# Performance work log

Measured on AMD Instinct MI355X. Metric: run time of the kernel, lower is better.

## Reference

```python
import jax, jax.numpy as jnp
import numpy as np

B, N, C = 4, 4096, 512
K = 683  # ceil(N / ratio=6.0)
TAU = 1.0
W_OCC, W_REP, W_ENT = 1.0, 0.1, 0.01
REP_TOPK, REP_MARGIN = 4, -1.0
NEG = -1e9


def setup_inputs() -> dict:
    key = jax.random.key(0)
    ks = jax.random.split(key, 5)
    s = jax.random.normal(ks[0], (B, N, C), jnp.float32)
    mu = jax.random.normal(ks[1], (B, N, 3), jnp.float32)
    # SPD covariance per residue: L L^T + 0.1 I
    L = jax.random.normal(ks[2], (B, N, 3, 3), jnp.float32) * 0.3
    Sigma = jnp.einsum('bnij,bnkj->bnik', L, L) + 0.1 * jnp.eye(3, dtype=jnp.float32)
    mask = jnp.ones((B, N), jnp.float32)
    W = jax.random.normal(ks[3], (C, C), jnp.float32) / np.sqrt(C).astype(np.float32)
    b = jnp.zeros((C,), jnp.float32)
    slots = jax.random.normal(ks[4], (K, C), jnp.float32) * 0.02
    return {"s": s, "mu": mu, "Sigma": Sigma, "mask": mask, "W": W, "b": b, "slots": slots}


def reference(s, mu, Sigma, mask, W, b, slots):
    Kk = slots.shape[0]
    # A = softmax((Linear(s)) . slots / tau), masked
    s_proj = jnp.einsum('bnc,dc->bnd', s, W) + b            # nn.Linear: x @ W^T + b
    logits = jnp.einsum('bnc,kc->bnk', s_proj, slots) / TAU
    logits = jnp.where((mask < 0.5)[..., None], NEG, logits)
    A = jax.nn.softmax(logits, axis=-1) * mask[..., None]   # [B,N,K]

    denom = jnp.maximum(A.sum(axis=1), 1e-8)                # [B,K]
    s_c = jnp.einsum('bnk,bnc->bkc', A, s) / denom[..., None]

    # moment-matching merge
    w = A / (A.sum(axis=1, keepdims=True) + 1e-8)           # [B,N,K]
    mu_c = jnp.einsum('bnk,bnd->bkd', w, mu)                # [B,K,3]
    intra = jnp.einsum('bnk,bnij->bkij', w, Sigma)          # [B,K,3,3]
    diff = mu[:, :, None, :] - mu_c[:, None, :, :]          # [B,N,K,3]
    inter = jnp.einsum('bnk,bnki,bnkj->bkij', w, diff, diff)
    Sigma_c = intra + inter                                 # [B,K,3,3]

    # occupancy balance loss
    occ = A.sum(axis=1)
    occ = occ / jnp.maximum(occ.sum(axis=-1, keepdims=True), 1e-8)
    loss_occ = jnp.mean((occ - 1.0 / Kk) ** 2)

    # repulsion loss (pairwise Gaussian overlap)
    delta = mu_c[:, :, None, :] - mu_c[:, None, :, :]       # [B,K,K,3]
    sig_sum = Sigma_c[:, :, None] + Sigma_c[:, None, :]     # [B,K,K,3,3]
    inv = jnp.linalg.inv(sig_sum + 1e-6 * jnp.eye(3, dtype=s.dtype))
    dist2 = jnp.einsum('bpqi,bpqij,bpqj->bpq', delta, inv, delta)
    score = -0.5 * dist2
    eye = jnp.eye(Kk, dtype=bool)[None]
    score = jnp.where(eye, NEG, score)
    top = jax.lax.top_k(score, min(REP_TOPK, Kk - 1))[0]
    loss_rep = jnp.mean(jax.nn.relu(top - REP_MARGIN))

    # entropy loss
    Ac = jnp.maximum(A, 1e-8)
    ent = -(Ac * jnp.log(Ac)).sum(axis=-1)                  # [B,N]
    loss_ent = (ent * mask).sum() / jnp.maximum(mask.sum(), 1.0)

    total = W_OCC * loss_occ + W_REP * loss_rep + W_ENT * loss_ent
    return (A, s_c, mu_c, Sigma_c, loss_occ, loss_rep, loss_ent, total)
```

## Files before the change

kernel.cpp:

```cpp
#include <hip/hip_runtime.h>
#include <math.h>

#define B_    4
#define N_    4096
#define C_    512
#define KSLOT 683

using bf16x8 = __attribute__((ext_vector_type(8))) short;
using f32x4  = __attribute__((ext_vector_type(4))) float;

#define OFF_A    0
#define OFF_SC   (B_*N_*KSLOT)
#define OFF_MU   (OFF_SC + B_*KSLOT*C_)
#define OFF_SIG  (OFF_MU + B_*KSLOT*3)
#define OFF_LOSS (OFF_SIG + B_*KSLOT*9)

#define WS_MOM    0
#define WS_INVMAX (WS_MOM + B_*KSLOT*16)
#define WS_OCCTB  (WS_INVMAX + B_*KSLOT)
#define WS_OCCT   (WS_OCCTB + 256)
#define WS_ENTB   (WS_OCCT + 4)
#define WS_MSB    (WS_ENTB + 256)
#define WS_OCCLB  (WS_MSB + 256)
#define WS_REPB   (WS_OCCLB + 256)
#define WS_BS     (WS_REPB + 256)
#define WS_FEND   (WS_BS + 704)

#define US_BASE  (WS_FEND*2)
#define US_SBF   US_BASE
#define US_STF   (US_SBF + B_*N_*C_)
#define US_WSL   (US_STF + B_*C_*N_)
#define US_FT    (US_WSL + 704*C_)
#define US_ATB   (US_FT + B_*16*N_)
#define US_END   (US_ATB + (size_t)B_*768*N_)


__device__ __forceinline__ ushort f2bf(float x) {
  union { float f; unsigned u; } v; v.f = x;
  unsigned r = v.u + 0x7fffu + ((v.u >> 16) & 1u);
  return (ushort)(r >> 16);
}

__device__ __forceinline__ float blockSum256(float v, float* red) {
#pragma unroll
  for (int off = 32; off; off >>= 1) v += __shfl_xor(v, off);
  __syncthreads();
  if ((threadIdx.x & 63) == 0) red[threadIdx.x >> 6] = v;
  __syncthreads();
  return red[0] + red[1] + red[2] + red[3];
}

__device__ __forceinline__ void top4_insert(float v, float& t0, float& t1, float& t2, float& t3) {
  if (v > t3) {
    if (v > t2) {
      t3 = t2;
      if (v > t1) {
        t2 = t1;
        if (v > t0) { t1 = t0; t0 = v; } else t1 = v;
      } else t2 = v;
    } else t3 = v;
  }
}

__global__ __launch_bounds__(256) void convert_s_kernel(const float* __restrict__ s,
                                                        ushort* __restrict__ sbf,
                                                        ushort* __restrict__ stf) {
  __shared__ float T[32][33];
  const int b = blockIdx.z;
  const int n0 = blockIdx.x * 32, c0 = blockIdx.y * 32;
  const int t = threadIdx.x;
  const int r = t >> 3, q4 = (t & 7) * 4;
  float4 v = *(const float4*)(s + ((size_t)(b * N_ + n0 + r)) * C_ + c0 + q4);
  ushort4 u;
  u.x = f2bf(v.x); u.y = f2bf(v.y); u.z = f2bf(v.z); u.w = f2bf(v.w);
  *(ushort4*)(sbf + ((size_t)(b * N_ + n0 + r)) * C_ + c0 + q4) = u;
  T[q4 + 0][r] = v.x; T[q4 + 1][r] = v.y; T[q4 + 2][r] = v.z; T[q4 + 3][r] = v.w;
  __syncthreads();
  ushort4 o;
  o.x = f2bf(T[r][q4 + 0]); o.y = f2bf(T[r][q4 + 1]);
  o.z = f2bf(T[r][q4 + 2]); o.w = f2bf(T[r][q4 + 3]);
  *(ushort4*)(stf + ((size_t)(b * C_ + c0 + r)) * N_ + n0 + q4) = o;
}

__global__ __launch_bounds__(256) void build_features_t(const float* __restrict__ mu,
                                                        const float* __restrict__ Sig,
                                                        ushort* __restrict__ ftg) {
  __shared__ ushort FT[16][272];
  const int t = threadIdx.x;
  const size_t ng = (size_t)blockIdx.x * 256 + t;
  const float* mp = mu + ng * 3;
  const float* sp = Sig + ng * 9;
  float m0 = mp[0], m1 = mp[1], m2 = mp[2];
  FT[0][t] = 0x3F80;
  FT[1][t] = f2bf(m0); FT[2][t] = f2bf(m1); FT[3][t] = f2bf(m2);
  FT[4][t] = f2bf(m0 * m0); FT[5][t] = f2bf(m0 * m1); FT[6][t] = f2bf(m0 * m2);
  FT[7][t] = f2bf(m1 * m1); FT[8][t] = f2bf(m1 * m2); FT[9][t] = f2bf(m2 * m2);
  FT[10][t] = f2bf(sp[0]); FT[11][t] = f2bf(sp[1]); FT[12][t] = f2bf(sp[2]);
  FT[13][t] = f2bf(sp[4]); FT[14][t] = f2bf(sp[5]); FT[15][t] = f2bf(sp[8]);
  __syncthreads();
  const int b = (int)((blockIdx.x * 256) >> 12);
  const int n0b = (blockIdx.x * 256) & (N_ - 1);
  for (int u = t; u < 512; u += 256) {
    int f = u >> 5, off = (u & 31) * 8;
    *(uint4*)(ftg + ((size_t)b * 16 + f) * N_ + n0b + off) = *(uint4*)(&FT[f][off]);
  }
}

__global__ __launch_bounds__(256) void wslots_bf16_kernel(const float* __restrict__ slots,
                                                          const float* __restrict__ W,
                                                          ushort* __restrict__ wsl) {
  __shared__ float SL[8][512];
  const int k0 = blockIdx.x * 8;
  const int c = blockIdx.y * 256 + threadIdx.x;
  for (int idx = threadIdx.x; idx < 8 * 512; idx += 256) {
    int kk = idx >> 9, d = idx & 511;
    SL[kk][d] = (k0 + kk < KSLOT) ? slots[(size_t)(k0 + kk) * C_ + d] : 0.f;
  }
  __syncthreads();
  float acc[8];
#pragma unroll
  for (int i = 0; i < 8; ++i) acc[i] = 0.f;
  for (int d = 0; d < C_; ++d) {
    float w = W[(size_t)d * C_ + c];
#pragma unroll
    for (int i = 0; i < 8; ++i) acc[i] += SL[i][d] * w;
  }
#pragma unroll
  for (int i = 0; i < 8; ++i)
    if (k0 + i < KSLOT) wsl[(size_t)(k0 + i) * C_ + c] = f2bf(acc[i]);
}

__global__ __launch_bounds__(256) void bs_kernel(const float* __restrict__ slots,
                                                 const float* __restrict__ bvec,
                                                 float* __restrict__ bs) {
  int k = blockIdx.x * 256 + threadIdx.x;
  if (k >= KSLOT) return;
  const float* srow = slots + (size_t)k * C_;
  float acc = 0.f;
  for (int d = 0; d < C_; ++d) acc += srow[d] * bvec[d];
  bs[k] = acc;
}

__device__ __forceinline__ void g1_epilogue(
    f32x4 (&acc)[11], const int rowbase, const int t, const int lane,
    const int rowg, const int colw,
    const float* __restrict__ bs, const float* __restrict__ mask,
    float* __restrict__ Aout, ushort* __restrict__ atb,
    float* __restrict__ entb, float* __restrict__ msb,
    float* Af, float (&red4)[32][4], const int binid) {
  __syncthreads();
  int cols[11]; bool valid[11];
#pragma unroll
  for (int cf = 0; cf < 11; ++cf) {
    cols[cf] = colw * 176 + cf * 16 + (lane & 15);
    valid[cf] = (cols[cf] < KSLOT);
    float bv = valid[cf] ? bs[cols[cf]] : 0.f;
#pragma unroll
    for (int r = 0; r < 4; ++r) acc[cf][r] += bv;
  }
  float m4[4];
#pragma unroll
  for (int r = 0; r < 4; ++r) m4[r] = -3.0e38f;
#pragma unroll
  for (int cf = 0; cf < 11; ++cf)
    if (valid[cf]) {
#pragma unroll
      for (int r = 0; r < 4; ++r) m4[r] = fmaxf(m4[r], acc[cf][r]);
    }
#pragma unroll
  for (int off = 1; off < 16; off <<= 1) {
#pragma unroll
    for (int r = 0; r < 4; ++r) m4[r] = fmaxf(m4[r], __shfl_xor(m4[r], off));
  }
  if ((lane & 15) == 0) {
#pragma unroll
    for (int r = 0; r < 4; ++r) red4[rowg * 16 + (lane >> 4) * 4 + r][colw] = m4[r];
  }
  __syncthreads();
#pragma unroll
  for (int r = 0; r < 4; ++r) {
    int rl = rowg * 16 + (lane >> 4) * 4 + r;
    m4[r] = fmaxf(fmaxf(red4[rl][0], red4[rl][1]), fmaxf(red4[rl][2], red4[rl][3]));
  }
  __syncthreads();
  float s4[4] = {0.f, 0.f, 0.f, 0.f};
#pragma unroll
  for (int cf = 0; cf < 11; ++cf)
    if (valid[cf]) {
#pragma unroll
      for (int r = 0; r < 4; ++r) {
        float e = __expf(acc[cf][r] - m4[r]);
        acc[cf][r] = e;
        s4[r] += e;
      }
    }
#pragma unroll
  for (int off = 1; off < 16; off <<= 1) {
#pragma unroll
    for (int r = 0; r < 4; ++r) s4[r] += __shfl_xor(s4[r], off);
  }
  if ((lane & 15) == 0) {
#pragma unroll
    for (int r = 0; r < 4; ++r) red4[rowg * 16 + (lane >> 4) * 4 + r][colw] = s4[r];
  }
  __syncthreads();
  float inv4[4], mr4[4];
#pragma unroll
  for (int r = 0; r < 4; ++r) {
    int rl = rowg * 16 + (lane >> 4) * 4 + r;
    float S = red4[rl][0] + red4[rl][1] + red4[rl][2] + red4[rl][3];
    inv4[r] = 1.f / S;
    mr4[r] = mask[rowbase + rl];
  }
  __syncthreads();
  float ent4[4] = {0.f, 0.f, 0.f, 0.f};
#pragma unroll
  for (int cf = 0; cf < 11; ++cf)
    if (valid[cf]) {
#pragma unroll
      for (int r = 0; r < 4; ++r) {
        int rl = rowg * 16 + (lane >> 4) * 4 + r;
        float a = acc[cf][r] * inv4[r] * mr4[r];
        Af[rl * KSLOT + cols[cf]] = a;
        float ac = fmaxf(a, 1e-8f);
        ent4[r] -= ac * __logf(ac);
      }
    }
#pragma unroll
  for (int off = 1; off < 16; off <<= 1) {
#pragma unroll
    for (int r = 0; r < 4; ++r) ent4[r] += __shfl_xor(ent4[r], off);
  }
  if ((lane & 15) == 0) {
#pragma unroll
    for (int r = 0; r < 4; ++r) red4[rowg * 16 + (lane >> 4) * 4 + r][colw] = ent4[r];
  }
  __syncthreads();
  if (t < 64) {
    float er = 0.f, ms = 0.f;
    if (t < 32) {
      float e = red4[t][0] + red4[t][1] + red4[t][2] + red4[t][3];
      float m = mask[rowbase + t];
      er = e * m; ms = m;
    }
#pragma unroll
    for (int off = 32; off; off >>= 1) { er += __shfl_xor(er, off); ms += __shfl_xor(ms, off); }
    if (t == 0) {
      atomicAdd(&entb[binid], er);
      atomicAdd(&msb[binid], ms);
    }
  }
  const float4* Af4 = (const float4*)Af;
  float4* Ag4 = (float4*)(Aout + (size_t)rowbase * KSLOT);
  for (int i = t; i < (32 * KSLOT) / 4; i += 512) Ag4[i] = Af4[i];
  {
    const int bb = rowbase >> 12;
    const int n0b = rowbase & (N_ - 1);
    ushort* Atb = atb + ((size_t)bb * 768) * N_ + n0b;
    for (int u = t; u < KSLOT * 4; u += 512) {
      int k = u >> 2, q = u & 3;
      ushort tmp[8];
#pragma unroll
      for (int j = 0; j < 8; ++j) tmp[j] = f2bf(Af[(q * 8 + j) * KSLOT + k]);
      *(uint4*)(Atb + (size_t)k * N_ + q * 8) = *(uint4*)tmp;
    }
  }
}

__global__ __launch_bounds__(512)
__attribute__((amdgpu_waves_per_eu(2, 2)))
void gemm1sm(const ushort* __restrict__ sbf,
             const ushort* __restrict__ wsl,
             const float* __restrict__ bs,
             const float* __restrict__ mask,
             float* __restrict__ Aout,
             ushort* __restrict__ atb,
             float* __restrict__ entb,
             float* __restrict__ msb) {
  __shared__ __align__(16) char SMEM[90112];
  float* Af = (float*)SMEM;
  __shared__ float red4[32][4];
  const int t = threadIdx.x;
  const int lane = t & 63;
  const int w = t >> 6;
  const int rowg = w >> 2;
  const int colw = w & 3;
  const int row0 = blockIdx.x * 64;
  const int r16 = rowg * 16 + (lane & 15);

  const ushort* arow0 = sbf + (size_t)(row0 + r16) * C_ + (lane >> 4) * 8;
  const ushort* arow1 = arow0 + (size_t)32 * C_;
  bf16x8 g0a = *(const bf16x8*)(arow0);
  bf16x8 g0b = *(const bf16x8*)(arow0 + 32);
  bf16x8 g1a = *(const bf16x8*)(arow1);
  bf16x8 g1b = *(const bf16x8*)(arow1 + 32);
  bf16x8 p0a, p0b, p1a, p1b;

  f32x4 acc0[11], acc1[11];
  f32x4 zero = {0.f, 0.f, 0.f, 0.f};
#pragma unroll
  for (int cf = 0; cf < 11; ++cf) { acc0[cf] = zero; acc1[cf] = zero; }

#pragma unroll
  for (int slab = 0; slab < 8; ++slab) {
    if (slab) __syncthreads();
#pragma unroll
    for (int i = 0; i < 11; ++i) {
      int idx = t + i * 512;
      int r = idx >> 3;
      int chs = (idx & 7) ^ (r & 7);
      const ushort* g = wsl + (size_t)r * C_ + slab * 64 + chs * 8;
      char* l = (char*)SMEM + i * 8192 + (t & 448) * 16;
      __builtin_amdgcn_global_load_lds(
          (const __attribute__((address_space(1))) void*)g,
          (__attribute__((address_space(3))) void*)l, 16, 0, 0);
    }
    __syncthreads();
    if (slab < 7) {
      p0a = *(const bf16x8*)(arow0 + (slab + 1) * 64);
      p0b = *(const bf16x8*)(arow0 + (slab + 1) * 64 + 32);
      p1a = *(const bf16x8*)(arow1 + (slab + 1) * 64);
      p1b = *(const bf16x8*)(arow1 + (slab + 1) * 64 + 32);
    }
    {
      const int ach0 = (lane >> 4);
#pragma unroll
      for (int cf = 0; cf < 11; ++cf) {
        int br = colw * 176 + cf * 16 + (lane & 15);
        bf16x8 bf = *(const bf16x8*)(SMEM + br * 128 + ((ach0 * 16) ^ ((br & 7) << 4)));
        acc0[cf] = __builtin_amdgcn_mfma_f32_16x16x32_bf16(g0a, bf, acc0[cf], 0, 0, 0);
        acc1[cf] = __builtin_amdgcn_mfma_f32_16x16x32_bf16(g1a, bf, acc1[cf], 0, 0, 0);
      }
      const int ach1 = 4 + (lane >> 4);
#pragma unroll
      for (int cf = 0; cf < 11; ++cf) {
        int br = colw * 176 + cf * 16 + (lane & 15);
        bf16x8 bf = *(const bf16x8*)(SMEM + br * 128 + ((ach1 * 16) ^ ((br & 7) << 4)));
        acc0[cf] = __builtin_amdgcn_mfma_f32_16x16x32_bf16(g0b, bf, acc0[cf], 0, 0, 0);
        acc1[cf] = __builtin_amdgcn_mfma_f32_16x16x32_bf16(g1b, bf, acc1[cf], 0, 0, 0);
      }
    }
    g0a = p0a; g0b = p0b; g1a = p1a; g1b = p1b;
  }

  g1_epilogue(acc0, row0, t, lane, rowg, colw, bs, mask, Aout, atb, entb, msb,
              Af, red4, (blockIdx.x * 2) & 255);
  g1_epilogue(acc1, row0 + 32, t, lane, rowg, colw, bs, mask, Aout, atb, entb, msb,
              Af, red4, (blockIdx.x * 2 + 1) & 255);
}

#define G2BUFB 18432
__global__ __launch_bounds__(256) void gemm2t(const ushort* __restrict__ atb,
                                              const ushort* __restrict__ stf,
                                              const ushort* __restrict__ ftg,
                                              float* __restrict__ sc,
                                              float* __restrict__ MOM) {
  __shared__ __align__(16) char LB[2 * G2BUFB];
  const int t = threadIdx.x;
  const int lane = t & 63;
  const int w = t >> 6;
  const int wm = w >> 1;
  const int wn = w & 1;
  const int fhw = blockIdx.x;
  const int logical = (fhw & 7) * 44 + (fhw >> 3);
  const int kt = logical % 11;
  const int ct = (logical / 11) & 7;
  const int b  = logical / 88;
  const bool do_mom = (ct == 0);
  const ushort* Ab = atb + ((size_t)b * 768 + kt * 64) * N_;
  const ushort* Sb = stf + ((size_t)b * C_ + ct * 64) * N_;
  const ushort* Fb = ftg + ((size_t)b * 16) * N_;

  f32x4 zero = {0.f, 0.f, 0.f, 0.f};
  f32x4 acc[2][2];
#pragma unroll
  for (int i = 0; i < 2; ++i)
#pragma unroll
    for (int j = 0; j < 2; ++j) acc[i][j] = zero;
  f32x4 accf[2];
#pragma unroll
  for (int i = 0; i < 2; ++i) accf[i] = zero;

#define G2_STAGE(BUFI, NB)                                                   \
  {                                                                          \
    char* AtL = LB + (BUFI) * G2BUFB;                                        \
    char* SsL = AtL + 8192;                                                  \
    char* FtL = AtL + 16384;                                                 \
    _Pragma("unroll")                                                        \
    for (int i = 0; i < 2; ++i) {                                            \
      int idx = t + i * 256;                                                 \
      int r = idx >> 3;                                                      \
      int chs = (idx & 7) ^ (r & 7);                                         \
      const ushort* g = Ab + (size_t)r * N_ + (NB) + chs * 8;                \
      char* l = AtL + i * 4096 + (t & 192) * 16;                             \
      __builtin_amdgcn_global_load_lds(                                      \
          (const __attribute__((address_space(1))) void*)g,                  \
          (__attribute__((address_space(3))) void*)l, 16, 0, 0);             \
    }                                                                        \
    _Pragma("unroll")                                                        \
    for (int i = 0; i < 2; ++i) {                                            \
      int idx = t + i * 256;                                                 \
      int r = idx >> 3;                                                      \
      int chs = (idx & 7) ^ (r & 7);                                         \
      const ushort* g = Sb + (size_t)r * N_ + (NB) + chs * 8;                \
      char* l = SsL + i * 4096 + (t & 192) * 16;                             \
      __builtin_amdgcn_global_load_lds(                                      \
          (const __attribute__((address_space(1))) void*)g,                  \
          (__attribute__((address_space(3))) void*)l, 16, 0, 0);             \
    }                                                                        \
    if (do_mom && t < 128) {                                                 \
      int idx = t;                                                           \
      int r = idx >> 3;                                                      \
      int chs = (idx & 7) ^ (r & 7);                                         \
      const ushort* g = Fb + (size_t)r * N_ + (NB) + chs * 8;                \
      char* l = FtL + (t & 192) * 16;                                        \
      __builtin_amdgcn_global_load_lds(                                      \
          (const __attribute__((address_space(1))) void*)g,                  \
          (__attribute__((address_space(3))) void*)l, 16, 0, 0);             \
    }                                                                        \
  }

  G2_STAGE(0, 0)
  for (int st = 0; st < 64; ++st) {
    const int cur = st & 1;
    __syncthreads();
    if (st < 63) G2_STAGE(cur ^ 1, (st + 1) * 64)
    char* AtL = LB + cur * G2BUFB;
    char* SsL = AtL + 8192;
    char* FtL = AtL + 16384;
#pragma unroll
    for (int ks2 = 0; ks2 < 2; ++ks2) {
      const int ach = ks2 * 4 + (lane >> 4);
      bf16x8 afr[2], bfr[2];
#pragma unroll
      for (int kf = 0; kf < 2; ++kf) {
        int ar = wm * 32 + kf * 16 + (lane & 15);
        afr[kf] = *(const bf16x8*)(AtL + ar * 128 + ((ach * 16) ^ ((ar & 7) << 4)));
      }
#pragma unroll
      for (int cg = 0; cg < 2; ++cg) {
        int br = wn * 32 + cg * 16 + (lane & 15);
        bfr[cg] = *(const bf16x8*)(SsL + br * 128 + ((ach * 16) ^ ((br & 7) << 4)));
      }
#pragma unroll
      for (int kf = 0; kf < 2; ++kf)
#pragma unroll
        for (int cg = 0; cg < 2; ++cg)
          acc[kf][cg] = __builtin_amdgcn_mfma_f32_16x16x32_bf16(afr[kf], bfr[cg], acc[kf][cg], 0, 0, 0);
      if (do_mom && wn == 0) {
        int fr = lane & 15;
        bf16x8 ffr = *(const bf16x8*)(FtL + fr * 128 + ((ach * 16) ^ ((fr & 7) << 4)));
#pragma unroll
        for (int kf = 0; kf < 2; ++kf)
          accf[kf] = __builtin_amdgcn_mfma_f32_16x16x32_bf16(afr[kf], ffr, accf[kf], 0, 0, 0);
      }
    }
  }
#undef G2_STAGE

#pragma unroll
  for (int kf = 0; kf < 2; ++kf) {
#pragma unroll
    for (int r = 0; r < 4; ++r) {
      int k = kt * 64 + wm * 32 + kf * 16 + (lane >> 4) * 4 + r;
      if (k >= KSLOT) continue;
      float* dst = sc + ((size_t)(b * KSLOT + k)) * C_ + ct * 64 + wn * 32;
#pragma unroll
      for (int cg = 0; cg < 2; ++cg)
        dst[cg * 16 + (lane & 15)] = acc[kf][cg][r];
    }
  }
  if (do_mom && wn == 0) {
#pragma unroll
    for (int kf = 0; kf < 2; ++kf) {
#pragma unroll
      for (int r = 0; r < 4; ++r) {
        int k = kt * 64 + wm * 32 + kf * 16 + (lane >> 4) * 4 + r;
        if (k >= KSLOT) continue;
        MOM[((size_t)b * KSLOT + k) * 16 + (lane & 15)] = accf[kf][r];
      }
    }
  }
}

__global__ __launch_bounds__(128) void scale_sc(float* __restrict__ sc,
                                                const float* __restrict__ invmax) {
  const int bk = blockIdx.x;
  const float sv = invmax[bk];
  float4* p = (float4*)(sc + (size_t)bk * C_);
  int t = threadIdx.x;
  float4 v = p[t];
  v.x *= sv; v.y *= sv; v.z *= sv; v.w *= sv;
  p[t] = v;
}

__global__ __launch_bounds__(256) void moments_kernel(const float* __restrict__ Amat,
                                                      const float* __restrict__ mu,
                                                      const float* __restrict__ Sig,
                                                      float* __restrict__ MOM) {
  __shared__ float red[64][17];
  const int b = blockIdx.z;
  const int kx = threadIdx.x & 63;
  const int k = blockIdx.x * 64 + kx;
  const int ng = threadIdx.x >> 6;
  const int n0 = blockIdx.y * 128;
  const bool valid = (k < KSLOT);

  float acc[16];
#pragma unroll
  for (int i = 0; i < 16; ++i) acc[i] = 0.f;

  const float* Abase = Amat + (size_t)b * N_ * KSLOT + k;
  const float* mubase = mu + ((size_t)b * N_) * 3;
  const float* sgbase = Sig + ((size_t)b * N_) * 9;

  for (int j = 0; j < 32; ++j) {
    const int n = n0 + ng + j * 4;
    float a = valid ? Abase[(size_t)n * KSLOT] : 0.f;
    const float* mp = mubase + (size_t)n * 3;
    const float* sp = sgbase + (size_t)n * 9;
    float m0 = mp[0], m1 = mp[1], m2 = mp[2];
    acc[0] += a;
    acc[1] += a * m0; acc[2] += a * m1; acc[3] += a * m2;
    acc[4] += a * m0 * m0; acc[5] += a * m0 * m1; acc[6] += a * m0 * m2;
    acc[7] += a * m1 * m1; acc[8] += a * m1 * m2; acc[9] += a * m2 * m2;
    acc[10] += a * sp[0]; acc[11] += a * sp[1]; acc[12] += a * sp[2];
    acc[13] += a * sp[4]; acc[14] += a * sp[5]; acc[15] += a * sp[8];
  }

  if (ng == 0) {
#pragma unroll
    for (int i = 0; i < 16; ++i) red[kx][i] = acc[i];
  }
  __syncthreads();
  if (ng == 1) {
#pragma unroll
    for (int i = 0; i < 16; ++i) red[kx][i] += acc[i];
  }
  __syncthreads();
  if (ng == 2) {
#pragma unroll
    for (int i = 0; i < 16; ++i) red[kx][i] += acc[i];
  }
  __syncthreads();
  if (ng == 3) {
#pragma unroll
    for (int i = 0; i < 16; ++i) red[kx][i] += acc[i];
  }
  __syncthreads();
  if (ng == 0 && valid) {
    float* dst = MOM + ((size_t)b * KSLOT + k) * 16;
#pragma unroll
    for (int i = 0; i < 16; ++i) atomicAdd(&dst[i], red[kx][i]);
  }
}

__global__ __launch_bounds__(256) void finalize_bk(const float* __restrict__ MOM,
                                                   float* __restrict__ muc,
                                                   float* __restrict__ sigc,
                                                   float* __restrict__ invmax,
                                                   float* __restrict__ occtb) {
  int bk = blockIdx.x * 256 + threadIdx.x;
  if (bk >= B_ * KSLOT) return;
  int b = bk / KSLOT;
  const float* T = MOM + (size_t)bk * 16;
  float den = T[0];
  float inv_eps = 1.f / (den + 1e-8f);
  float inv_mx = 1.f / fmaxf(den, 1e-8f);
  float mc0 = T[1] * inv_eps, mc1 = T[2] * inv_eps, mc2 = T[3] * inv_eps;
  float M0 = den * inv_eps;
  float cf = 2.f - M0;
  float S00 = (T[10] + T[4]) * inv_eps - cf * mc0 * mc0;
  float S01 = (T[11] + T[5]) * inv_eps - cf * mc0 * mc1;
  float S02 = (T[12] + T[6]) * inv_eps - cf * mc0 * mc2;
  float S11 = (T[13] + T[7]) * inv_eps - cf * mc1 * mc1;
  float S12 = (T[14] + T[8]) * inv_eps - cf * mc1 * mc2;
  float S22 = (T[15] + T[9]) * inv_eps - cf * mc2 * mc2;
  muc[(size_t)bk * 3 + 0] = mc0;
  muc[(size_t)bk * 3 + 1] = mc1;
  muc[(size_t)bk * 3 + 2] = mc2;
  float* sg = sigc + (size_t)bk * 9;
  sg[0] = S00; sg[1] = S01; sg[2] = S02;
  sg[3] = S01; sg[4] = S11; sg[5] = S12;
  sg[6] = S02; sg[7] = S12; sg[8] = S22;
  invmax[bk] = inv_mx;
  atomicAdd(&occtb[b * 64 + (threadIdx.x & 63)], den);
}

__global__ void reduce_occT(const float* __restrict__ bins, float* __restrict__ occT) {
  int tid = threadIdx.x;
  float v = bins[tid];
#pragma unroll
  for (int off = 32; off; off >>= 1) v += __shfl_xor(v, off);
  if ((tid & 63) == 0) occT[tid >> 6] = v;
}

__global__ __launch_bounds__(256) void occ_loss_kernel(const float* __restrict__ MOM,
                                                       const float* __restrict__ occT,
                                                       float* __restrict__ occlb) {
  __shared__ float red[4];
  int bk = blockIdx.x * 256 + threadIdx.x;
  float d2 = 0.f;
  if (bk < B_ * KSLOT) {
    int b = bk / KSLOT;
    float den = MOM[(size_t)bk * 16];
    float occ = den / fmaxf(occT[b], 1e-8f);
    float d = occ - (1.f / (float)KSLOT);
    d2 = d * d;
  }
  float ssum = blockSum256(d2, red);
  if (threadIdx.x == 0) occlb[blockIdx.x] = ssum;
}

__global__ __launch_bounds__(256) void repulsion_kernel2(const float* __restrict__ muc,
                                                         const float* __restrict__ sigc,
                                                         float* __restrict__ repb) {
  __shared__ float L[KSLOT * 13];
  const int b = blockIdx.y;
  const int t = threadIdx.x;
  const float* mb = muc + (size_t)b * KSLOT * 3;
  const float* sb = sigc + (size_t)b * KSLOT * 9;
  for (int idx = t; idx < KSLOT * 3; idx += 256) {
    int r = idx / 3, c = idx - r * 3;
    L[r * 13 + c] = mb[idx];
  }
  for (int idx = t; idx < KSLOT * 9; idx += 256) {
    int r = idx / 9, c = idx - r * 9;
    L[r * 13 + 3 + c] = sb[idx];
  }
  __syncthreads();
  const int w = t >> 6, lane = t & 63;
  const int p = blockIdx.x * 4 + w;
  if (p >= KSLOT) return;
  const float* Lp = L + p * 13;
  const float mp0 = Lp[0], mp1 = Lp[1], mp2 = Lp[2];
  const float pa = Lp[3], pb = Lp[4], pc = Lp[5], pd = Lp[7], pe = Lp[8], pf = Lp[11];
  float t0 = -3e38f, t1 = -3e38f, t2 = -3e38f, t3 = -3e38f;
  for (int q = lane; q < KSLOT; q += 64) {
    if (q == p) continue;
    const float* Lq = L + q * 13;
    float d0 = mp0 - Lq[0];
    float d1 = mp1 - Lq[1];
    float d2 = mp2 - Lq[2];
    float a  = pa + Lq[3] + 1e-6f;
    float bb = pb + Lq[4];
    float cc = pc + Lq[5];
    float d  = pd + Lq[7] + 1e-6f;
    float e  = pe + Lq[8];
    float f  = pf + Lq[11] + 1e-6f;
    float C00 = d * f - e * e;
    float C01 = cc * e - bb * f;
    float C02 = bb * e - cc * d;
    float C11 = a * f - cc * cc;
    float C12 = bb * cc - a * e;
    float C22 = a * d - bb * bb;
    float det = a * C00 + bb * C01 + cc * C02;
    float dist2 = (C00 * d0 * d0 + C11 * d1 * d1 + C22 * d2 * d2 +
                   2.f * (C01 * d0 * d1 + C02 * d0 * d2 + C12 * d1 * d2)) / det;
    top4_insert(-0.5f * dist2, t0, t1, t2, t3);
  }
#pragma unroll
  for (int off = 1; off < 64; off <<= 1) {
    float u0 = __shfl_xor(t0, off);
    float u1 = __shfl_xor(t1, off);
    float u2 = __shfl_xor(t2, off);
    float u3 = __shfl_xor(t3, off);
    top4_insert(u0, t0, t1, t2, t3);
    top4_insert(u1, t0, t1, t2, t3);
    top4_insert(u2, t0, t1, t2, t3);
    top4_insert(u3, t0, t1, t2, t3);
  }
  if (lane == 0) {
    float s = fmaxf(t0 + 1.f, 0.f) + fmaxf(t1 + 1.f, 0.f) +
              fmaxf(t2 + 1.f, 0.f) + fmaxf(t3 + 1.f, 0.f);
    atomicAdd(&repb[(b * KSLOT + p) & 255], s);
  }
}

__global__ __launch_bounds__(256) void final_scalars(const float* __restrict__ entb,
                                                     const float* __restrict__ msb,
                                                     const float* __restrict__ occlb,
                                                     const float* __restrict__ repb,
                                                     float* __restrict__ out) {
  __shared__ float red[4];
  int tid = threadIdx.x;
  float e = blockSum256(entb[tid], red);
  float ms = blockSum256(msb[tid], red);
  float oc = blockSum256(occlb[tid], red);
  float rp = blockSum256(repb[tid], red);
  if (tid == 0) {
    float loss_ent = e / fmaxf(ms, 1.f);
    float loss_occ = oc / (float)(B_ * KSLOT);
    float loss_rep = rp / (float)(B_ * KSLOT * 4);
    out[0] = loss_occ;
    out[1] = loss_rep;
    out[2] = loss_ent;
    out[3] = 1.0f * loss_occ + 0.1f * loss_rep + 0.01f * loss_ent;
  }
}


__global__ __launch_bounds__(256) void wslots_kernel(const float* __restrict__ slots,
                                                     const float* __restrict__ W,
                                                     float* __restrict__ Wsl) {
  int k = blockIdx.x;
  int c = blockIdx.y * 256 + threadIdx.x;
  const float* srow = slots + (size_t)k * C_;
  float acc = 0.f;
  for (int d = 0; d < C_; d += 4) {
    acc += srow[d] * W[(size_t)d * C_ + c];
    acc += srow[d + 1] * W[(size_t)(d + 1) * C_ + c];
    acc += srow[d + 2] * W[(size_t)(d + 2) * C_ + c];
    acc += srow[d + 3] * W[(size_t)(d + 3) * C_ + c];
  }
  Wsl[(size_t)k * C_ + c] = acc;
}

__global__ __launch_bounds__(256) void softmax_rows(float* __restrict__ Amat,
                                                    const float* __restrict__ mask,
                                                    float* __restrict__ entb,
                                                    float* __restrict__ msb) {
  __shared__ float red[4];
  const int row = blockIdx.x;
  const int tid = threadIdx.x;
  float* rowp = Amat + (size_t)row * KSLOT;
  const float m = mask[row];
  const bool msk = (m < 0.5f);
  float v[3];
#pragma unroll
  for (int i = 0; i < 3; ++i) {
    int k = tid + i * 256;
    if (k < KSLOT) {
      float l = rowp[k];
      v[i] = msk ? -1e9f : l;
    } else v[i] = -3.0e38f;
  }
  float lmax = fmaxf(fmaxf(v[0], v[1]), v[2]);
#pragma unroll
  for (int off = 32; off; off >>= 1) lmax = fmaxf(lmax, __shfl_xor(lmax, off));
  __syncthreads();
  if ((tid & 63) == 0) red[tid >> 6] = lmax;
  __syncthreads();
  lmax = fmaxf(fmaxf(red[0], red[1]), fmaxf(red[2], red[3]));
  float lsum = 0.f;
#pragma unroll
  for (int i = 0; i < 3; ++i) {
    int k = tid + i * 256;
    float e = (k < KSLOT) ? expf(v[i] - lmax) : 0.f;
    v[i] = e;
    lsum += e;
  }
  lsum = blockSum256(lsum, red);
  float inv = 1.f / lsum;
  float ent = 0.f;
#pragma unroll
  for (int i = 0; i < 3; ++i) {
    int k = tid + i * 256;
    if (k < KSLOT) {
      float a = v[i] * inv * m;
      rowp[k] = a;
      float ac = fmaxf(a, 1e-8f);
      ent -= ac * logf(ac);
    }
  }
  ent = blockSum256(ent, red);
  if (tid == 0) {
    int bin = blockIdx.x & 255;
    atomicAdd(&entb[bin], ent * m);
    atomicAdd(&msb[bin], m);
  }
}

__global__ __launch_bounds__(256) void gemm_nt(const float* __restrict__ Am,
                                               const float* __restrict__ Bm,
                                               const float* __restrict__ bias,
                                               float* __restrict__ Cm,
                                               int M, int Nout, int Kd,
                                               int lda, int ldb, int ldc) {
  __shared__ float As[16][132];
  __shared__ float Bs[16][132];
  const int tid = threadIdx.x;
  const int tx = tid & 15, ty = tid >> 4;
  const int m0 = blockIdx.x * 128, n0 = blockIdx.y * 128;
  float acc[8][8];
#pragma unroll
  for (int i = 0; i < 8; ++i)
#pragma unroll
    for (int j = 0; j < 8; ++j) acc[i][j] = 0.f;
  const int r = tid >> 1, hc = (tid & 1) * 8;
  for (int k0 = 0; k0 < Kd; k0 += 16) {
    float va[8], vb[8];
    int gm = m0 + r;
    if (gm < M) {
      const float* p = Am + (size_t)gm * lda + k0 + hc;
      *(float4*)(va) = *(const float4*)(p);
      *(float4*)(va + 4) = *(const float4*)(p + 4);
    } else {
#pragma unroll
      for (int i = 0; i < 8; ++i) va[i] = 0.f;
    }
    int gn = n0 + r;
    if (gn < Nout) {
      const float* p = Bm + (size_t)gn * ldb + k0 + hc;
      *(float4*)(vb) = *(const float4*)(p);
      *(float4*)(vb + 4) = *(const float4*)(p + 4);
    } else {
#pragma unroll
      for (int i = 0; i < 8; ++i) vb[i] = 0.f;
    }
#pragma unroll
    for (int i = 0; i < 8; ++i) As[hc + i][r] = va[i];
#pragma unroll
    for (int i = 0; i < 8; ++i) Bs[hc + i][r] = vb[i];
    __syncthreads();
#pragma unroll
    for (int kk = 0; kk < 16; ++kk) {
      float a[8], bb[8];
      *(float4*)(a) = *(const float4*)&As[kk][ty * 8];
      *(float4*)(a + 4) = *(const float4*)&As[kk][ty * 8 + 4];
      *(float4*)(bb) = *(const float4*)&Bs[kk][tx * 8];
      *(float4*)(bb + 4) = *(const float4*)&Bs[kk][tx * 8 + 4];
#pragma unroll
      for (int i = 0; i < 8; ++i)
#pragma unroll
        for (int j = 0; j < 8; ++j) acc[i][j] += a[i] * bb[j];
    }
    __syncthreads();
  }
#pragma unroll
  for (int i = 0; i < 8; ++i) {
    int gm = m0 + ty * 8 + i;
    if (gm >= M) continue;
    float* crow = Cm + (size_t)gm * ldc;
#pragma unroll
    for (int j = 0; j < 8; ++j) {
      int gn = n0 + tx * 8 + j;
      if (gn < Nout) crow[gn] = acc[i][j] + bias[gn];
    }
  }
}

__global__ __launch_bounds__(256) void gemm_tn(const float* __restrict__ Aall,
                                               const float* __restrict__ Ball,
                                               const float* __restrict__ scale,
                                               float* __restrict__ Call) {
  const int b = blockIdx.z;
  const float* Am = Aall + (size_t)b * N_ * KSLOT;
  const float* Bv = Ball + (size_t)b * N_ * C_;
  float* Cm = Call + (size_t)b * KSLOT * C_;
  const float* sc = scale + (size_t)b * KSLOT;
  __shared__ float As[16][132];
  __shared__ float Bs[16][68];
  const int tid = threadIdx.x;
  const int tx = tid & 15, ty = tid >> 4;
  const int m0 = blockIdx.x * 128, n0 = blockIdx.y * 64;
  float acc[8][4];
#pragma unroll
  for (int i = 0; i < 8; ++i)
#pragma unroll
    for (int j = 0; j < 4; ++j) acc[i][j] = 0.f;
  const int rr = tid >> 4;
  const int mq = tid & 15;
  const int cq = (tid & 15) * 4;
  for (int r0 = 0; r0 < N_; r0 += 16) {
#pragma unroll
    for (int i = 0; i < 8; ++i) {
      int mm = mq + 16 * i;
      int gm = m0 + mm;
      As[rr][mm] = (gm < KSLOT) ? Am[(size_t)(r0 + rr) * KSLOT + gm] : 0.f;
    }
    *(float4*)&Bs[rr][cq] = *(const float4*)(Bv + (size_t)(r0 + rr) * C_ + n0 + cq);
    __syncthreads();
#pragma unroll
    for (int kk = 0; kk < 16; ++kk) {
      float a[8], bb[4];
      *(float4*)(a) = *(const float4*)&As[kk][ty * 8];
      *(float4*)(a + 4) = *(const float4*)&As[kk][ty * 8 + 4];
      *(float4*)(bb) = *(const float4*)&Bs[kk][tx * 4];
#pragma unroll
      for (int i = 0; i < 8; ++i)
#pragma unroll
        for (int j = 0; j < 4; ++j) acc[i][j] += a[i] * bb[j];
    }
    __syncthreads();
  }
#pragma unroll
  for (int i = 0; i < 8; ++i) {
    int gm = m0 + ty * 8 + i;
    if (gm < KSLOT) {
      float s = sc[gm];
      float4 v;
      v.x = acc[i][0] * s; v.y = acc[i][1] * s; v.z = acc[i][2] * s; v.w = acc[i][3] * s;
      *(float4*)(Cm + (size_t)gm * C_ + n0 + tx * 4) = v;
    }
  }
}

extern "C" void kernel_launch(void* const* d_in, const int* in_sizes, int n_in,
                              void* d_out, int out_size, void* d_ws, size_t ws_size,
                              hipStream_t stream) {
  const float* s     = (const float*)d_in[0];
  const float* mu    = (const float*)d_in[1];
  const float* Sig   = (const float*)d_in[2];
  const float* mask  = (const float*)d_in[3];
  const float* W     = (const float*)d_in[4];
  const float* bvec  = (const float*)d_in[5];
  const float* slots = (const float*)d_in[6];
  float* out = (float*)d_out;
  float* ws  = (float*)d_ws;

  float* Amat = out + OFF_A;
  const bool fast = (ws_size >= (size_t)US_END * 2 + 64);

  (void)hipMemsetAsync(ws, 0, WS_FEND * sizeof(float), stream);
  bs_kernel<<<dim3(3), 256, 0, stream>>>(slots, bvec, ws + WS_BS);

  if (fast) {
    ushort* usw = (ushort*)ws;
    ushort* sbf = usw + US_SBF;
    ushort* stf = usw + US_STF;
    ushort* wsl = usw + US_WSL;
    ushort* ftg = usw + US_FT;
    ushort* atb = usw + US_ATB;

    convert_s_kernel<<<dim3(N_ / 32, C_ / 32, B_), 256, 0, stream>>>(s, sbf, stf);
    build_features_t<<<dim3(B_ * N_ / 256), 256, 0, stream>>>(mu, Sig, ftg);
    wslots_bf16_kernel<<<dim3((KSLOT + 7) / 8, C_ / 256), 256, 0, stream>>>(slots, W, wsl);

    gemm1sm<<<dim3(B_ * N_ / 64), 512, 0, stream>>>(
        sbf, wsl, ws + WS_BS, mask, Amat, atb, ws + WS_ENTB, ws + WS_MSB);

    gemm2t<<<dim3(352), 256, 0, stream>>>(
        atb, stf, ftg, out + OFF_SC, ws + WS_MOM);

    finalize_bk<<<dim3((B_ * KSLOT + 255) / 256), 256, 0, stream>>>(
        ws + WS_MOM, out + OFF_MU, out + OFF_SIG, ws + WS_INVMAX, ws + WS_OCCTB);

    reduce_occT<<<dim3(1), 256, 0, stream>>>(ws + WS_OCCTB, ws + WS_OCCT);
    occ_loss_kernel<<<dim3((B_ * KSLOT + 255) / 256), 256, 0, stream>>>(
        ws + WS_MOM, ws + WS_OCCT, ws + WS_OCCLB);

    scale_sc<<<dim3(B_ * KSLOT), 128, 0, stream>>>(out + OFF_SC, ws + WS_INVMAX);

    repulsion_kernel2<<<dim3((KSLOT + 3) / 4, B_), 256, 0, stream>>>(
        out + OFF_MU, out + OFF_SIG, ws + WS_REPB);

    final_scalars<<<dim3(1), 256, 0, stream>>>(
        ws + WS_ENTB, ws + WS_MSB, ws + WS_OCCLB, ws + WS_REPB, out + OFF_LOSS);
  } else {
    float* Wsl = out + OFF_SC;

    wslots_kernel<<<dim3(KSLOT, 2), 256, 0, stream>>>(slots, W, Wsl);
    gemm_nt<<<dim3((B_ * N_) / 128, (KSLOT + 127) / 128), 256, 0, stream>>>(
        s, Wsl, ws + WS_BS, Amat, B_ * N_, KSLOT, C_, C_, C_, KSLOT);
    softmax_rows<<<dim3(B_ * N_), 256, 0, stream>>>(Amat, mask, ws + WS_ENTB, ws + WS_MSB);
    moments_kernel<<<dim3(11, N_ / 128, B_), 256, 0, stream>>>(
        Amat, mu, Sig, ws + WS_MOM);
    finalize_bk<<<dim3((B_ * KSLOT + 255) / 256), 256, 0, stream>>>(
        ws + WS_MOM, out + OFF_MU, out + OFF_SIG, ws + WS_INVMAX, ws + WS_OCCTB);
    reduce_occT<<<dim3(1), 256, 0, stream>>>(ws + WS_OCCTB, ws + WS_OCCT);
    occ_loss_kernel<<<dim3((B_ * KSLOT + 255) / 256), 256, 0, stream>>>(
        ws + WS_MOM, ws + WS_OCCT, ws + WS_OCCLB);
    gemm_tn<<<dim3((KSLOT + 127) / 128, C_ / 64, B_), 256, 0, stream>>>(
        Amat, s, ws + WS_INVMAX, out + OFF_SC);
    repulsion_kernel2<<<dim3((KSLOT + 3) / 4, B_), 256, 0, stream>>>(
        out + OFF_MU, out + OFF_SIG, ws + WS_REPB);
    final_scalars<<<dim3(1), 256, 0, stream>>>(
        ws + WS_ENTB, ws + WS_MSB, ws + WS_OCCLB, ws + WS_REPB, out + OFF_LOSS);
  }
}
```

Before: 193.3 us.

## Fold slot-denominator scaling into gemm2t and stage A tile in bf16 LDS

The softmax epilogue of the first GEMM now accumulates per-slot column sums of A and adds them atomically into a workspace denominator. A small kernel inverts these sums, and gemm2t applies the scale in its store epilogue, so the separate scale_sc pass over s_c goes away. The epilogue also stages both 32-row halves of A in LDS as bf16 and writes A and its transpose in a single combined pass. The side effect is that the returned fp32 A is now bf16-rounded, which may break output accuracy, and the column sums add atomic traffic.

Result: slower. 216.0 us (+11.8%).

```diff
diff --git a/kernel.cpp b/kernel.cpp
--- a/kernel.cpp
+++ b/kernel.cpp
@@ -24,7 +24,8 @@
 #define WS_OCCLB  (WS_MSB + 256)
 #define WS_REPB   (WS_OCCLB + 256)
 #define WS_BS     (WS_REPB + 256)
-#define WS_FEND   (WS_BS + 704)
+#define WS_DEN    (WS_BS + 704)
+#define WS_FEND   (WS_DEN + B_*KSLOT)
 
 #define US_BASE  (WS_FEND*2)
 #define US_SBF   US_BASE
@@ -39,6 +40,11 @@
   union { float f; unsigned u; } v; v.f = x;
   unsigned r = v.u + 0x7fffu + ((v.u >> 16) & 1u);
   return (ushort)(r >> 16);
+}
+
+__device__ __forceinline__ float bf2f(ushort x) {
+  union { unsigned u; float f; } v; v.u = ((unsigned)x) << 16;
+  return v.f;
 }
 
 __device__ __forceinline__ float blockSum256(float v, float* red) {
@@ -141,13 +147,13 @@
   bs[k] = acc;
 }
 
-__device__ __forceinline__ void g1_epilogue(
+__device__ __forceinline__ void g1_epi_compute(
     f32x4 (&acc)[11], const int rowbase, const int t, const int lane,
     const int rowg, const int colw,
     const float* __restrict__ bs, const float* __restrict__ mask,
-    float* __restrict__ Aout, ushort* __restrict__ atb,
     float* __restrict__ entb, float* __restrict__ msb,
-    float* Af, float (&red4)[32][4], const int binid) {
+    float* __restrict__ denb,
+    ushort* Afg, float (&red4)[32][4], const int binid) {
   __syncthreads();
   int cols[11]; bool valid[11];
 #pragma unroll
@@ -214,6 +220,9 @@
   }
   __syncthreads();
   float ent4[4] = {0.f, 0.f, 0.f, 0.f};
+  float csum[11];
+#pragma unroll
+  for (int cf = 0; cf < 11; ++cf) csum[cf] = 0.f;
 #pragma unroll
   for (int cf = 0; cf < 11; ++cf)
     if (valid[cf]) {
@@ -221,9 +230,10 @@
       for (int r = 0; r < 4; ++r) {
         int rl = rowg * 16 + (lane >> 4) * 4 + r;
         float a = acc[cf][r] * inv4[r] * mr4[r];
-        Af[rl * KSLOT + cols[cf]] = a;
+        Afg[rl * KSLOT + cols[cf]] = f2bf(a);
         float ac = fmaxf(a, 1e-8f);
         ent4[r] -= ac * __logf(ac);
+        csum[cf] += a;
       }
     }
 #pragma unroll
@@ -250,20 +260,13 @@
       atomicAdd(&msb[binid], ms);
     }
   }
-  const float4* Af4 = (const float4*)Af;
-  float4* Ag4 = (float4*)(Aout + (size_t)rowbase * KSLOT);
-  for (int i = t; i < (32 * KSLOT) / 4; i += 512) Ag4[i] = Af4[i];
-  {
-    const int bb = rowbase >> 12;
-    const int n0b = rowbase & (N_ - 1);
-    ushort* Atb = atb + ((size_t)bb * 768) * N_ + n0b;
-    for (int u = t; u < KSLOT * 4; u += 512) {
-      int k = u >> 2, q = u & 3;
-      ushort tmp[8];
-#pragma unroll
-      for (int j = 0; j < 8; ++j) tmp[j] = f2bf(Af[(q * 8 + j) * KSLOT + k]);
-      *(uint4*)(Atb + (size_t)k * N_ + q * 8) = *(uint4*)tmp;
-    }
+#pragma unroll
+  for (int cf = 0; cf < 11; ++cf) {
+    float v = csum[cf];
+    v += __shfl_xor(v, 16);
+    v += __shfl_xor(v, 32);
+    if ((lane & 63) < 16 && valid[cf])
+      atomicAdd(&denb[cols[cf]], v);
   }
 }
 
@@ -276,9 +279,9 @@
              float* __restrict__ Aout,
              ushort* __restrict__ atb,
              float* __restrict__ entb,
-             float* __restrict__ msb) {
+             float* __restrict__ msb,
+             float* __restrict__ den) {
   __shared__ __align__(16) char SMEM[90112];
-  float* Af = (float*)SMEM;
   __shared__ float red4[32][4];
   const int t = threadIdx.x;
   const int lane = t & 63;
@@ -287,6 +290,7 @@
   const int colw = w & 3;
   const int row0 = blockIdx.x * 64;
   const int r16 = rowg * 16 + (lane & 15);
+  const int bb = row0 >> 12;
 
   const ushort* arow0 = sbf + (size_t)(row0 + r16) * C_ + (lane >> 4) * 8;
   const ushort* arow1 = arow0 + (size_t)32 * C_;
@@ -343,16 +347,47 @@
     g0a = p0a; g0b = p0b; g1a = p1a; g1b = p1b;
   }
 
-  g1_epilogue(acc0, row0, t, lane, rowg, colw, bs, mask, Aout, atb, entb, msb,
-              Af, red4, (blockIdx.x * 2) & 255);
-  g1_epilogue(acc1, row0 + 32, t, lane, rowg, colw, bs, mask, Aout, atb, entb, msb,
-              Af, red4, (blockIdx.x * 2 + 1) & 255);
+  ushort* Af0 = (ushort*)SMEM;
+  ushort* Af1 = (ushort*)SMEM + 32 * KSLOT;
+  float* denb = den + bb * KSLOT;
+  g1_epi_compute(acc0, row0, t, lane, rowg, colw, bs, mask, entb, msb, denb,
+                 Af0, red4, (blockIdx.x * 2) & 255);
+  g1_epi_compute(acc1, row0 + 32, t, lane, rowg, colw, bs, mask, entb, msb, denb,
+                 Af1, red4, (blockIdx.x * 2 + 1) & 255);
+  __syncthreads();
+
+  const ushort* Afu = (const ushort*)SMEM;
+  float* Ag = Aout + (size_t)row0 * KSLOT;
+  for (int i = t; i < (64 * KSLOT) / 4; i += 512) {
+    ushort4 u = *(const ushort4*)(Afu + i * 4);
+    float4 v;
+    v.x = bf2f(u.x); v.y = bf2f(u.y); v.z = bf2f(u.z); v.w = bf2f(u.w);
+    *(float4*)(Ag + i * 4) = v;
+  }
+  {
+    const int n0b = row0 & (N_ - 1);
+    ushort* Atb = atb + ((size_t)bb * 768) * N_ + n0b;
+    for (int u = t; u < KSLOT * 8; u += 512) {
+      int k = u >> 3, q = u & 7;
+      ushort tmp[8];
+#pragma unroll
+      for (int j = 0; j < 8; ++j) tmp[j] = Afu[(q * 8 + j) * KSLOT + k];
+      *(uint4*)(Atb + (size_t)k * N_ + q * 8) = *(uint4*)tmp;
+    }
+  }
+}
+
+__global__ __launch_bounds__(256) void inv_den(const float* __restrict__ den,
+                                               float* __restrict__ invmax) {
+  int bk = blockIdx.x * 256 + threadIdx.x;
+  if (bk < B_ * KSLOT) invmax[bk] = 1.f / fmaxf(den[bk], 1e-8f);
 }
 
 #define G2BUFB 18432
 __global__ __launch_bounds__(256) void gemm2t(const ushort* __restrict__ atb,
                                               const ushort* __restrict__ stf,
                                               const ushort* __restrict__ ftg,
+                                              const float* __restrict__ invmax,
                                               float* __restrict__ sc,
                                               float* __restrict__ MOM) {
   __shared__ __align__(16) char LB[2 * G2BUFB];
@@ -464,10 +499,11 @@
     for (int r = 0; r < 4; ++r) {
       int k = kt * 64 + wm * 32 + kf * 16 + (lane >> 4) * 4 + r;
       if (k >= KSLOT) continue;
+      float sv = invmax[b * KSLOT + k];
       float* dst = sc + ((size_t)(b * KSLOT + k)) * C_ + ct * 64 + wn * 32;
 #pragma unroll
       for (int cg = 0; cg < 2; ++cg)
-        dst[cg * 16 + (lane & 15)] = acc[kf][cg][r];
+        dst[cg * 16 + (lane & 15)] = acc[kf][cg][r] * sv;
     }
   }
   if (do_mom && wn == 0) {
@@ -481,17 +517,6 @@
       }
     }
   }
-}
-
-__global__ __launch_bounds__(128) void scale_sc(float* __restrict__ sc,
-                                                const float* __restrict__ invmax) {
-  const int bk = blockIdx.x;
-  const float sv = invmax[bk];
-  float4* p = (float4*)(sc + (size_t)bk * C_);
-  int t = threadIdx.x;
-  float4 v = p[t];
-  v.x *= sv; v.y *= sv; v.z *= sv; v.w *= sv;
-  p[t] = v;
 }
 
 __global__ __launch_bounds__(256) void moments_kernel(const float* __restrict__ Amat,
@@ -928,10 +953,13 @@
     wslots_bf16_kernel<<<dim3((KSLOT + 7) / 8, C_ / 256), 256, 0, stream>>>(slots, W, wsl);
 
     gemm1sm<<<dim3(B_ * N_ / 64), 512, 0, stream>>>(
-        sbf, wsl, ws + WS_BS, mask, Amat, atb, ws + WS_ENTB, ws + WS_MSB);
+        sbf, wsl, ws + WS_BS, mask, Amat, atb, ws + WS_ENTB, ws + WS_MSB, ws + WS_DEN);
+
+    inv_den<<<dim3((B_ * KSLOT + 255) / 256), 256, 0, stream>>>(
+        ws + WS_DEN, ws + WS_INVMAX);
 
     gemm2t<<<dim3(352), 256, 0, stream>>>(
-        atb, stf, ftg, out + OFF_SC, ws + WS_MOM);
+        atb, stf, ftg, ws + WS_INVMAX, out + OFF_SC, ws + WS_MOM);
 
     finalize_bk<<<dim3((B_ * KSLOT + 255) / 256), 256, 0, stream>>>(
         ws + WS_MOM, out + OFF_MU, out + OFF_SIG, ws + WS_INVMAX, ws + WS_OCCTB);
@@ -939,8 +967,6 @@
     reduce_occT<<<dim3(1), 256, 0, stream>>>(ws + WS_OCCTB, ws + WS_OCCT);
     occ_loss_kernel<<<dim3((B_ * KSLOT + 255) / 256), 256, 0, stream>>>(
         ws + WS_MOM, ws + WS_OCCT, ws + WS_OCCLB);
-
-    scale_sc<<<dim3(B_ * KSLOT), 128, 0, stream>>>(out + OFF_SC, ws + WS_INVMAX);
 
     repulsion_kernel2<<<dim3((KSLOT + 3) / 4, B_), 256, 0, stream>>>(
         out + OFF_MU, out + OFF_SIG, ws + WS_REPB);
```
